# Kernel tuning notes

Measured on AMD Instinct MI355X. Metric: run time of the kernel, lower is better.

The kernel has to match this reference:

```python
import jax, jax.numpy as jnp
import numpy as np

B, NA, NK, E = 128, 1024, 10, 768
EPS = 1e-7


def setup_inputs() -> dict:
    k0 = jax.random.key(0)
    k1, k2, k3, k4 = jax.random.split(k0, 4)
    ans = jax.random.normal(k1, (B, NA, E), dtype=jnp.float32)
    key = jax.random.normal(k2, (B, NK, E), dtype=jnp.float32)
    # 0/1 padding masks; guarantee at least one valid token per row
    mask_ans = (jax.random.uniform(k3, (B, NA)) < 0.9).astype(jnp.float32)
    mask_ans = mask_ans.at[:, 0].set(1.0)
    mask_key = (jax.random.uniform(k4, (B, NK)) < 0.9).astype(jnp.float32)
    mask_key = mask_key.at[:, 0].set(1.0)
    return {"ans": ans, "mask_ans": mask_ans, "key": key, "mask_key": mask_key}


def reference(ans, mask_ans, key, mask_key):
    # additive -inf biases for padded positions, shaped [B,1,N]
    mask_ans_inf = (jnp.abs(mask_ans - 1.0) * -10000.0)[:, None, :]  # [B,1,NA]
    mask_key_inf = (jnp.abs(mask_key - 1.0) * -10000.0)[:, None, :]  # [B,1,NK]
    ans = ans * mask_ans[:, :, None]
    key = key * mask_key[:, :, None]

    # op == 'dp': raw dot-product scores, key x ans^T -> [B,NK,NA]
    Z = jnp.einsum('bke,bae->bka', key, ans)

    # cosine-normalized scores (intended math of the repeat_interleave/reshape)
    norm_ans = jnp.sqrt(jnp.maximum(jnp.sum(ans * ans, -1), EPS))  # [B,NA]
    norm_key = jnp.sqrt(jnp.maximum(jnp.sum(key * key, -1), EPS))  # [B,NK]
    Z_cos = Z / (norm_key[:, :, None] * norm_ans[:, None, :])      # [B,NK,NA]

    # key-direction attention: softmax over NK, aggregate key tokens per ans token
    Z_softmax_key = jax.nn.softmax(jnp.swapaxes(Z, 1, 2) + mask_key_inf, axis=2)  # [B,NA,NK]
    V = jnp.einsum('bak,bke->bae', Z_softmax_key, key) * mask_ans[:, :, None]     # [B,NA,E]

    # ans-direction attention: softmax over NA, aggregate ans tokens per key token
    Z_softmax_ans = jax.nn.softmax(Z + mask_ans_inf, axis=2)                      # [B,NK,NA]
    U = jnp.einsum('bka,bae->bke', Z_softmax_ans, ans) * mask_key[:, :, None]     # [B,NK,E]

    # sigmoid gating from best cosine match (temperature 5)
    beta_key = jax.nn.sigmoid(jnp.max(Z_cos + mask_ans_inf, axis=2) * 5.0)[:, :, None]  # [B,NK,1]
    beta_ans = jax.nn.sigmoid(
        jnp.max(jnp.swapaxes(Z_cos, 1, 2) + mask_key_inf, axis=2) * 5.0)[:, :, None]    # [B,NA,1]

    # beta == True
    U = U * beta_key
    V = V * beta_ans

    # word_att_pool == 'max'
    u = jnp.max(U, axis=1)  # [B,E]
    v = jnp.max(V, axis=1)  # [B,E]

    # merge_ans_key == 'concat'
    f = jnp.concatenate([u, v], axis=1)  # [B,2E]

    return (f, Z, Z_softmax_ans,
            jnp.swapaxes(Z_softmax_key, 1, 2),  # [B,NK,NA]
            jnp.swapaxes(beta_ans, 1, 2),       # [B,1,NA]
            jnp.swapaxes(beta_key, 1, 2))       # [B,1,NK]
```

## Files before the change

### kernel.cpp

```cpp
#include <hip/hip_runtime.h>
#include <math.h>

#define NB 128
#define NA 1024
#define NK 10
#define EDIM 768
#define NS 4
#define CHUNK (NA/NS)
#define WPB 4
#define TPB 256
#define TPW (CHUNK/WPB)
#define NG (TPW/4)
#define EPSV 1e-7f

#define F_OFF   0
#define Z_OFF   196608
#define ZSA_OFF 1507328
#define ZSK_OFF 2818048
#define BA_OFF  4128768
#define BK_OFF  4259840

#define WS_META (NK*EDIM + EDIM)
#define WS_STRIDE (WS_META + 32)

__device__ __forceinline__ float wave_sum(float v) {
#define DPPADD(ctrl) v += __int_as_float(__builtin_amdgcn_update_dpp(0, __float_as_int(v), ctrl, 0xf, 0xf, true))
  DPPADD(0x111); DPPADD(0x112); DPPADD(0x114); DPPADD(0x118);
  DPPADD(0x142); DPPADD(0x143);
#undef DPPADD
  return __int_as_float(__builtin_amdgcn_readlane(__float_as_int(v), 63));
}

__global__ __launch_bounds__(TPB, 1) void kv_pass1(
    const float* __restrict__ ans, const float* __restrict__ mask_ans,
    const float* __restrict__ key, const float* __restrict__ mask_key,
    float* __restrict__ out, float* __restrict__ ws)
{
  const int s = blockIdx.x, b = blockIdx.y;
  const int tid = threadIdx.x;
  const int lane = tid & 63, wave = tid >> 6;

  __shared__ float key_s[NK][EDIM];
  __shared__ float red_u[NK][EDIM];
  __shared__ float vred[WPB][EDIM];
  __shared__ float rnk_s[NK], mki_s[NK];
  __shared__ float shm[WPB][NK], shl[WPB][NK], shmc[WPB][NK];
  __shared__ float fm[NK];

  {
    const float* kb = key + (size_t)b*NK*EDIM;
    float* kd = &key_s[0][0];
    for (int i = tid*4; i < NK*EDIM; i += TPB*4) {
      float4 v = *(const float4*)(kb + i);
      float mk = mask_key[b*NK + (i / EDIM)];
      v.x*=mk; v.y*=mk; v.z*=mk; v.w*=mk;
      *(float4*)(kd + i) = v;
    }
  }
  __syncthreads();
  for (int k = wave; k < NK; k += WPB) {
    float ss = 0.f;
    for (int j = lane; j < EDIM; j += 64) { float t = key_s[k][j]; ss += t*t; }
    ss = wave_sum(ss);
    if (lane == 0) {
      rnk_s[k] = rsqrtf(fmaxf(ss, EPSV));
      mki_s[k] = (mask_key[b*NK + k] - 1.0f) * 10000.0f;
    }
  }
  __syncthreads();

  float Uacc[NK][12];
  float vmax[12];
  float m[NK], l[NK], mc[NK];
#pragma unroll
  for (int k = 0; k < NK; ++k) {
    m[k] = -1e30f; l[k] = 0.f; mc[k] = -3e38f;
#pragma unroll
    for (int j = 0; j < 12; ++j) Uacc[k][j] = 0.f;
  }
#pragma unroll
  for (int j = 0; j < 12; ++j) vmax[j] = -3e38f;

  const float* ansb = ans + (size_t)b*NA*EDIM;
  const int abase = s*CHUNK + wave*TPW;

#pragma unroll 1
  for (int g = 0; g < NG; ++g) {
    const int a0 = abase + g*4;
    float av[4][12];
    float ma[4], mainf[4], rna[4], bfac[4];
    float zz[4][NK];

#pragma unroll
    for (int t = 0; t < 4; ++t) {
      const int a = a0 + t;
      const float mav = mask_ans[b*NA + a];
      ma[t] = mav; mainf[t] = (mav - 1.0f)*10000.0f;
      float ns = 0.f;
#pragma unroll
      for (int j = 0; j < 3; ++j) {
        float4 v = *(const float4*)(ansb + (size_t)a*EDIM + j*256 + lane*4);
        v.x*=mav; v.y*=mav; v.z*=mav; v.w*=mav;
        av[t][j*4+0]=v.x; av[t][j*4+1]=v.y; av[t][j*4+2]=v.z; av[t][j*4+3]=v.w;
        ns += v.x*v.x + v.y*v.y + v.z*v.z + v.w*v.w;
      }
      ns = wave_sum(ns);
      rna[t] = rsqrtf(fmaxf(ns, EPSV));
    }

#pragma unroll
    for (int k = 0; k < NK; ++k) {
      float kb0[12];
#pragma unroll
      for (int j = 0; j < 3; ++j) {
        float4 v = *(const float4*)(&key_s[k][j*256 + lane*4]);
        kb0[j*4+0]=v.x; kb0[j*4+1]=v.y; kb0[j*4+2]=v.z; kb0[j*4+3]=v.w;
      }
#pragma unroll
      for (int t = 0; t < 4; ++t) {
        float p = 0.f;
#pragma unroll
        for (int j = 0; j < 12; ++j) p += av[t][j]*kb0[j];
        zz[t][k] = p;
      }
    }
#pragma unroll
    for (int t = 0; t < 4; ++t)
#pragma unroll
      for (int k = 0; k < NK; ++k) zz[t][k] = wave_sum(zz[t][k]);

    float w[4][NK];
#pragma unroll
    for (int t = 0; t < 4; ++t) {
      const int a = a0 + t;
      {
        float zv = zz[t][0];
#pragma unroll
        for (int k = 1; k < NK; ++k) zv = (lane == k) ? zz[t][k] : zv;
        if (lane < NK) out[Z_OFF + ((size_t)b*NK + lane)*NA + a] = zv;
      }
      float mk = zz[t][0] + mki_s[0];
#pragma unroll
      for (int k = 1; k < NK; ++k) mk = fmaxf(mk, zz[t][k] + mki_s[k]);
      float sum = 0.f;
#pragma unroll
      for (int k = 0; k < NK; ++k) { float e = __expf(zz[t][k] + mki_s[k] - mk); w[t][k] = e; sum += e; }
      float rs = 1.0f / sum;
#pragma unroll
      for (int k = 0; k < NK; ++k) w[t][k] *= rs;
      {
        float wv = w[t][0];
#pragma unroll
        for (int k = 1; k < NK; ++k) wv = (lane == k) ? w[t][k] : wv;
        if (lane < NK) out[ZSK_OFF + ((size_t)b*NK + lane)*NA + a] = wv;
      }
      float zc0 = zz[t][0]*rnk_s[0]*rna[t];
      float cb = zc0 + mki_s[0];
      mc[0] = fmaxf(mc[0], zc0 + mainf[t]);
#pragma unroll
      for (int k = 1; k < NK; ++k) {
        float zc = zz[t][k]*rnk_s[k]*rna[t];
        cb = fmaxf(cb, zc + mki_s[k]);
        mc[k] = fmaxf(mc[k], zc + mainf[t]);
      }
      float beta = 1.0f / (1.0f + __expf(-5.0f*cb));
      if (lane == 0) out[BA_OFF + (size_t)b*NA + a] = beta;
      bfac[t] = beta * ma[t];
#pragma unroll
      for (int k = 0; k < NK; ++k) {
        float sc = zz[t][k] + mainf[t];
        if (sc > m[k]) {
          float scale = __expf(m[k] - sc);
          m[k] = sc; l[k] *= scale;
#pragma unroll
          for (int j = 0; j < 12; ++j) Uacc[k][j] *= scale;
        }
        float p = __expf(sc - m[k]);
        l[k] += p;
#pragma unroll
        for (int j = 0; j < 12; ++j) Uacc[k][j] += p * av[t][j];
      }
    }

    float Vv[4][12];
#pragma unroll
    for (int t = 0; t < 4; ++t)
#pragma unroll
      for (int j = 0; j < 12; ++j) Vv[t][j] = 0.f;
#pragma unroll
    for (int k = 0; k < NK; ++k) {
      float kb0[12];
#pragma unroll
      for (int j = 0; j < 3; ++j) {
        float4 v = *(const float4*)(&key_s[k][j*256 + lane*4]);
        kb0[j*4+0]=v.x; kb0[j*4+1]=v.y; kb0[j*4+2]=v.z; kb0[j*4+3]=v.w;
      }
#pragma unroll
      for (int t = 0; t < 4; ++t)
#pragma unroll
        for (int j = 0; j < 12; ++j) Vv[t][j] += w[t][k]*kb0[j];
    }
#pragma unroll
    for (int t = 0; t < 4; ++t)
#pragma unroll
      for (int j = 0; j < 12; ++j) vmax[j] = fmaxf(vmax[j], Vv[t][j]*bfac[t]);
  }

  if (lane == 0) {
#pragma unroll
    for (int k = 0; k < NK; ++k) { shm[wave][k]=m[k]; shl[wave][k]=l[k]; shmc[wave][k]=mc[k]; }
  }
#pragma unroll
  for (int j = 0; j < 12; ++j) vred[wave][(j>>2)*256 + lane*4 + (j&3)] = vmax[j];
  for (int i = tid; i < NK*EDIM; i += TPB) (&red_u[0][0])[i] = 0.f;
  __syncthreads();

  float* wsb = ws + (size_t)(b*NS + s)*WS_STRIDE;
  if (tid < NK) {
    const int k = tid;
    float M = shm[0][k];
#pragma unroll
    for (int w2 = 1; w2 < WPB; ++w2) M = fmaxf(M, shm[w2][k]);
    float L = 0.f, MC = shmc[0][k];
#pragma unroll
    for (int w2 = 0; w2 < WPB; ++w2) {
      L += shl[w2][k]*__expf(shm[w2][k]-M);
      MC = fmaxf(MC, shmc[w2][k]);
    }
    fm[k] = M;
    wsb[WS_META + k] = M;
    wsb[WS_META + NK + k] = L;
    wsb[WS_META + 2*NK + k] = MC;
  }
  __syncthreads();
#pragma unroll
  for (int k = 0; k < NK; ++k) {
    float fw = __expf(m[k] - fm[k]);
#pragma unroll
    for (int j = 0; j < 12; ++j)
      atomicAdd(&red_u[k][(j>>2)*256 + lane*4 + (j&3)], fw*Uacc[k][j]);
  }
  __syncthreads();
  for (int i = tid; i < NK*EDIM; i += TPB) wsb[i] = (&red_u[0][0])[i];
  for (int i = tid; i < EDIM; i += TPB)
    wsb[NK*EDIM + i] = fmaxf(fmaxf(vred[0][i], vred[1][i]), fmaxf(vred[2][i], vred[3][i]));
}

__global__ __launch_bounds__(256, 1) void kv_pass2(
    const float* __restrict__ mask_ans, const float* __restrict__ mask_key,
    float* __restrict__ out, const float* __restrict__ ws)
{
  const int b = blockIdx.x, tid = threadIdx.x;
  __shared__ float shM[NK], shRL[NK], shFac[NK], shF[NS][NK];
  if (tid < NK) {
    const int k = tid;
    const float* w0 = ws + (size_t)(b*NS)*WS_STRIDE + WS_META;
    float M = w0[k];
#pragma unroll
    for (int s2 = 1; s2 < NS; ++s2) M = fmaxf(M, w0[(size_t)s2*WS_STRIDE + k]);
    float L = 0.f, MC = -3e38f;
#pragma unroll
    for (int s2 = 0; s2 < NS; ++s2) {
      float ms = w0[(size_t)s2*WS_STRIDE + k];
      float f = __expf(ms - M);
      shF[s2][k] = f;
      L  += w0[(size_t)s2*WS_STRIDE + NK + k] * f;
      MC  = fmaxf(MC, w0[(size_t)s2*WS_STRIDE + 2*NK + k]);
    }
    float bk = 1.0f/(1.0f + __expf(-5.0f*MC));
    out[BK_OFF + b*NK + k] = bk;
    float rl = 1.0f / L;
    shM[k] = M; shRL[k] = rl;
    shFac[k] = rl * mask_key[b*NK + k] * bk;
  }
  __syncthreads();
  const float* wsb = ws + (size_t)(b*NS)*WS_STRIDE;
#pragma unroll 1
  for (int e = tid; e < EDIM; e += 256) {
    float u = -3e38f;
#pragma unroll
    for (int k = 0; k < NK; ++k) {
      float acc = 0.f;
#pragma unroll
      for (int s2 = 0; s2 < NS; ++s2) acc += shF[s2][k] * wsb[(size_t)s2*WS_STRIDE + k*EDIM + e];
      u = fmaxf(u, acc * shFac[k]);
    }
    out[(size_t)b*(2*EDIM) + e] = u;
    float v = wsb[NK*EDIM + e];
#pragma unroll
    for (int s2 = 1; s2 < NS; ++s2) v = fmaxf(v, wsb[(size_t)s2*WS_STRIDE + NK*EDIM + e]);
    out[(size_t)b*(2*EDIM) + EDIM + e] = v;
  }
  for (int i = tid; i < NK*NA; i += 256) {
    const int a = i & (NA-1);
    const int k = i >> 10;
    float z = out[Z_OFF + (size_t)b*NK*NA + i];
    float mainf = (mask_ans[b*NA + a] - 1.0f) * 10000.0f;
    out[ZSA_OFF + (size_t)b*NK*NA + i] = __expf(z + mainf - shM[k]) * shRL[k];
  }
}

extern "C" void kernel_launch(void* const* d_in, const int* in_sizes, int n_in,
                              void* d_out, int out_size, void* d_ws, size_t ws_size,
                              hipStream_t stream) {
  const float* ans      = (const float*)d_in[0];
  const float* mask_ans = (const float*)d_in[1];
  const float* key      = (const float*)d_in[2];
  const float* mask_key = (const float*)d_in[3];
  float* out = (float*)d_out;
  float* ws  = (float*)d_ws;

  dim3 g1(NS, NB);
  kv_pass1<<<g1, TPB, 0, stream>>>(ans, mask_ans, key, mask_key, out, ws);
  kv_pass2<<<NB, 256, 0, stream>>>(mask_ans, mask_key, out, ws);
}
```

Measured before the change: 1.467 ms.

## Move ans-direction softmax aggregation out of online loop into separate third pass

```diff
diff --git a/kernel.cpp b/kernel.cpp
--- a/kernel.cpp
+++ b/kernel.cpp
@@ -10,7 +10,6 @@
 #define WPB 4
 #define TPB 256
 #define TPW (CHUNK/WPB)
-#define NG (TPW/4)
 #define EPSV 1e-7f
 
 #define F_OFF   0
@@ -20,8 +19,10 @@
 #define BA_OFF  4128768
 #define BK_OFF  4259840
 
-#define WS_META (NK*EDIM + EDIM)
-#define WS_STRIDE (WS_META + 32)
+#define WS_RNK 0
+#define WS_RNA (WS_RNK + NB*NK)
+#define WS_VP  (WS_RNA + NB*NA)
+#define WS_FAC (WS_VP + NB*NS*EDIM)
 
 __device__ __forceinline__ float wave_sum(float v) {
 #define DPPADD(ctrl) v += __int_as_float(__builtin_amdgcn_update_dpp(0, __float_as_int(v), ctrl, 0xf, 0xf, true))
@@ -30,8 +31,15 @@
 #undef DPPADD
   return __int_as_float(__builtin_amdgcn_readlane(__float_as_int(v), 63));
 }
-
-__global__ __launch_bounds__(TPB, 1) void kv_pass1(
+__device__ __forceinline__ float wave_max(float v) {
+#define DPPMAX(ctrl) { float o_ = __int_as_float(__builtin_amdgcn_update_dpp(__float_as_int(v), __float_as_int(v), ctrl, 0xf, 0xf, false)); v = fmaxf(v, o_); }
+  DPPMAX(0x111) DPPMAX(0x112) DPPMAX(0x114) DPPMAX(0x118)
+  DPPMAX(0x142) DPPMAX(0x143)
+#undef DPPMAX
+  return __int_as_float(__builtin_amdgcn_readlane(__float_as_int(v), 63));
+}
+
+__global__ __launch_bounds__(TPB, 2) void kv_pass1(
     const float* __restrict__ ans, const float* __restrict__ mask_ans,
     const float* __restrict__ key, const float* __restrict__ mask_key,
     float* __restrict__ out, float* __restrict__ ws)
@@ -41,43 +49,33 @@
   const int lane = tid & 63, wave = tid >> 6;
 
   __shared__ float key_s[NK][EDIM];
-  __shared__ float red_u[NK][EDIM];
   __shared__ float vred[WPB][EDIM];
   __shared__ float rnk_s[NK], mki_s[NK];
-  __shared__ float shm[WPB][NK], shl[WPB][NK], shmc[WPB][NK];
-  __shared__ float fm[NK];
 
   {
     const float* kb = key + (size_t)b*NK*EDIM;
-    float* kd = &key_s[0][0];
     for (int i = tid*4; i < NK*EDIM; i += TPB*4) {
       float4 v = *(const float4*)(kb + i);
       float mk = mask_key[b*NK + (i / EDIM)];
       v.x*=mk; v.y*=mk; v.z*=mk; v.w*=mk;
-      *(float4*)(kd + i) = v;
+      *(float4*)(&key_s[0][0] + i) = v;
     }
   }
   __syncthreads();
   for (int k = wave; k < NK; k += WPB) {
-    float ss = 0.f;
-    for (int j = lane; j < EDIM; j += 64) { float t = key_s[k][j]; ss += t*t; }
-    ss = wave_sum(ss);
+    float ssum = 0.f;
+    for (int j = lane; j < EDIM; j += 64) { float t = key_s[k][j]; ssum += t*t; }
+    ssum = wave_sum(ssum);
     if (lane == 0) {
-      rnk_s[k] = rsqrtf(fmaxf(ss, EPSV));
+      float r = rsqrtf(fmaxf(ssum, EPSV));
+      rnk_s[k] = r;
       mki_s[k] = (mask_key[b*NK + k] - 1.0f) * 10000.0f;
-    }
-  }
-  __syncthreads();
-
-  float Uacc[NK][12];
+      if (s == 0) ws[WS_RNK + b*NK + k] = r;
+    }
+  }
+  __syncthreads();
+
   float vmax[12];
-  float m[NK], l[NK], mc[NK];
-#pragma unroll
-  for (int k = 0; k < NK; ++k) {
-    m[k] = -1e30f; l[k] = 0.f; mc[k] = -3e38f;
-#pragma unroll
-    for (int j = 0; j < 12; ++j) Uacc[k][j] = 0.f;
-  }
 #pragma unroll
   for (int j = 0; j < 12; ++j) vmax[j] = -3e38f;
 
@@ -85,17 +83,16 @@
   const int abase = s*CHUNK + wave*TPW;
 
 #pragma unroll 1
-  for (int g = 0; g < NG; ++g) {
-    const int a0 = abase + g*4;
-    float av[4][12];
-    float ma[4], mainf[4], rna[4], bfac[4];
-    float zz[4][NK];
-
-#pragma unroll
-    for (int t = 0; t < 4; ++t) {
+  for (int g = 0; g < TPW/2; ++g) {
+    const int a0 = abase + g*2;
+    float av[2][12], rna2[2], ma2[2], bfac[2];
+    float zz[2][NK], w[2][NK];
+
+#pragma unroll
+    for (int t = 0; t < 2; ++t) {
       const int a = a0 + t;
       const float mav = mask_ans[b*NA + a];
-      ma[t] = mav; mainf[t] = (mav - 1.0f)*10000.0f;
+      ma2[t] = mav;
       float ns = 0.f;
 #pragma unroll
       for (int j = 0; j < 3; ++j) {
@@ -105,43 +102,40 @@
         ns += v.x*v.x + v.y*v.y + v.z*v.z + v.w*v.w;
       }
       ns = wave_sum(ns);
-      rna[t] = rsqrtf(fmaxf(ns, EPSV));
+      rna2[t] = rsqrtf(fmaxf(ns, EPSV));
+      if (lane == 0) ws[WS_RNA + b*NA + a] = rna2[t];
     }
 
 #pragma unroll
     for (int k = 0; k < NK; ++k) {
-      float kb0[12];
+      float kr[12];
 #pragma unroll
       for (int j = 0; j < 3; ++j) {
         float4 v = *(const float4*)(&key_s[k][j*256 + lane*4]);
-        kb0[j*4+0]=v.x; kb0[j*4+1]=v.y; kb0[j*4+2]=v.z; kb0[j*4+3]=v.w;
-      }
-#pragma unroll
-      for (int t = 0; t < 4; ++t) {
-        float p = 0.f;
-#pragma unroll
-        for (int j = 0; j < 12; ++j) p += av[t][j]*kb0[j];
-        zz[t][k] = p;
-      }
-    }
-#pragma unroll
-    for (int t = 0; t < 4; ++t)
+        kr[j*4+0]=v.x; kr[j*4+1]=v.y; kr[j*4+2]=v.z; kr[j*4+3]=v.w;
+      }
+      float p0 = 0.f, p1 = 0.f;
+#pragma unroll
+      for (int j = 0; j < 12; ++j) { p0 += av[0][j]*kr[j]; p1 += av[1][j]*kr[j]; }
+      zz[0][k] = p0; zz[1][k] = p1;
+    }
+#pragma unroll
+    for (int t = 0; t < 2; ++t)
 #pragma unroll
       for (int k = 0; k < NK; ++k) zz[t][k] = wave_sum(zz[t][k]);
 
-    float w[4][NK];
-#pragma unroll
-    for (int t = 0; t < 4; ++t) {
+#pragma unroll
+    for (int t = 0; t < 2; ++t) {
       const int a = a0 + t;
       {
         float zv = zz[t][0];
 #pragma unroll
         for (int k = 1; k < NK; ++k) zv = (lane == k) ? zz[t][k] : zv;
-        if (lane < NK) out[Z_OFF + ((size_t)b*NK + lane)*NA + a] = zv;
-      }
-      float mk = zz[t][0] + mki_s[0];
-#pragma unroll
-      for (int k = 1; k < NK; ++k) mk = fmaxf(mk, zz[t][k] + mki_s[k]);
+        if (lane < NK) out[Z_OFF + ((size_t)(b*NK) + lane)*NA + a] = zv;
+      }
+      float mk = -3e38f;
+#pragma unroll
+      for (int k = 0; k < NK; ++k) mk = fmaxf(mk, zz[t][k] + mki_s[k]);
       float sum = 0.f;
 #pragma unroll
       for (int k = 0; k < NK; ++k) { float e = __expf(zz[t][k] + mki_s[k] - mk); w[t][k] = e; sum += e; }
@@ -152,152 +146,133 @@
         float wv = w[t][0];
 #pragma unroll
         for (int k = 1; k < NK; ++k) wv = (lane == k) ? w[t][k] : wv;
-        if (lane < NK) out[ZSK_OFF + ((size_t)b*NK + lane)*NA + a] = wv;
-      }
-      float zc0 = zz[t][0]*rnk_s[0]*rna[t];
-      float cb = zc0 + mki_s[0];
-      mc[0] = fmaxf(mc[0], zc0 + mainf[t]);
-#pragma unroll
-      for (int k = 1; k < NK; ++k) {
-        float zc = zz[t][k]*rnk_s[k]*rna[t];
-        cb = fmaxf(cb, zc + mki_s[k]);
-        mc[k] = fmaxf(mc[k], zc + mainf[t]);
-      }
+        if (lane < NK) out[ZSK_OFF + ((size_t)(b*NK) + lane)*NA + a] = wv;
+      }
+      float cb = -3e38f;
+#pragma unroll
+      for (int k = 0; k < NK; ++k) cb = fmaxf(cb, zz[t][k]*rnk_s[k]*rna2[t] + mki_s[k]);
       float beta = 1.0f / (1.0f + __expf(-5.0f*cb));
       if (lane == 0) out[BA_OFF + (size_t)b*NA + a] = beta;
-      bfac[t] = beta * ma[t];
-#pragma unroll
-      for (int k = 0; k < NK; ++k) {
-        float sc = zz[t][k] + mainf[t];
-        if (sc > m[k]) {
-          float scale = __expf(m[k] - sc);
-          m[k] = sc; l[k] *= scale;
-#pragma unroll
-          for (int j = 0; j < 12; ++j) Uacc[k][j] *= scale;
-        }
-        float p = __expf(sc - m[k]);
-        l[k] += p;
-#pragma unroll
-        for (int j = 0; j < 12; ++j) Uacc[k][j] += p * av[t][j];
-      }
-    }
-
-    float Vv[4][12];
-#pragma unroll
-    for (int t = 0; t < 4; ++t)
+      bfac[t] = beta * ma2[t];
+    }
+
+    float Vv[2][12];
+#pragma unroll
+    for (int t = 0; t < 2; ++t)
 #pragma unroll
       for (int j = 0; j < 12; ++j) Vv[t][j] = 0.f;
 #pragma unroll
     for (int k = 0; k < NK; ++k) {
-      float kb0[12];
+      float kr[12];
 #pragma unroll
       for (int j = 0; j < 3; ++j) {
         float4 v = *(const float4*)(&key_s[k][j*256 + lane*4]);
-        kb0[j*4+0]=v.x; kb0[j*4+1]=v.y; kb0[j*4+2]=v.z; kb0[j*4+3]=v.w;
-      }
-#pragma unroll
-      for (int t = 0; t < 4; ++t)
-#pragma unroll
-        for (int j = 0; j < 12; ++j) Vv[t][j] += w[t][k]*kb0[j];
-    }
-#pragma unroll
-    for (int t = 0; t < 4; ++t)
+        kr[j*4+0]=v.x; kr[j*4+1]=v.y; kr[j*4+2]=v.z; kr[j*4+3]=v.w;
+      }
+#pragma unroll
+      for (int t = 0; t < 2; ++t)
+#pragma unroll
+        for (int j = 0; j < 12; ++j) Vv[t][j] += w[t][k]*kr[j];
+    }
+#pragma unroll
+    for (int t = 0; t < 2; ++t)
 #pragma unroll
       for (int j = 0; j < 12; ++j) vmax[j] = fmaxf(vmax[j], Vv[t][j]*bfac[t]);
   }
 
-  if (lane == 0) {
-#pragma unroll
-    for (int k = 0; k < NK; ++k) { shm[wave][k]=m[k]; shl[wave][k]=l[k]; shmc[wave][k]=mc[k]; }
-  }
-#pragma unroll
-  for (int j = 0; j < 12; ++j) vred[wave][(j>>2)*256 + lane*4 + (j&3)] = vmax[j];
-  for (int i = tid; i < NK*EDIM; i += TPB) (&red_u[0][0])[i] = 0.f;
-  __syncthreads();
-
-  float* wsb = ws + (size_t)(b*NS + s)*WS_STRIDE;
-  if (tid < NK) {
-    const int k = tid;
-    float M = shm[0][k];
-#pragma unroll
-    for (int w2 = 1; w2 < WPB; ++w2) M = fmaxf(M, shm[w2][k]);
-    float L = 0.f, MC = shmc[0][k];
-#pragma unroll
-    for (int w2 = 0; w2 < WPB; ++w2) {
-      L += shl[w2][k]*__expf(shm[w2][k]-M);
-      MC = fmaxf(MC, shmc[w2][k]);
-    }
-    fm[k] = M;
-    wsb[WS_META + k] = M;
-    wsb[WS_META + NK + k] = L;
-    wsb[WS_META + 2*NK + k] = MC;
-  }
-  __syncthreads();
-#pragma unroll
-  for (int k = 0; k < NK; ++k) {
-    float fw = __expf(m[k] - fm[k]);
-#pragma unroll
-    for (int j = 0; j < 12; ++j)
-      atomicAdd(&red_u[k][(j>>2)*256 + lane*4 + (j&3)], fw*Uacc[k][j]);
-  }
-  __syncthreads();
-  for (int i = tid; i < NK*EDIM; i += TPB) wsb[i] = (&red_u[0][0])[i];
+#pragma unroll
+  for (int j = 0; j < 3; ++j)
+    *(float4*)(&vred[wave][j*256 + lane*4]) =
+      make_float4(vmax[j*4+0], vmax[j*4+1], vmax[j*4+2], vmax[j*4+3]);
+  __syncthreads();
   for (int i = tid; i < EDIM; i += TPB)
-    wsb[NK*EDIM + i] = fmaxf(fmaxf(vred[0][i], vred[1][i]), fmaxf(vred[2][i], vred[3][i]));
-}
-
-__global__ __launch_bounds__(256, 1) void kv_pass2(
+    ws[WS_VP + ((size_t)(b*NS + s))*EDIM + i] =
+      fmaxf(fmaxf(vred[0][i], vred[1][i]), fmaxf(vred[2][i], vred[3][i]));
+}
+
+__global__ __launch_bounds__(256, 2) void kv_pass2(
     const float* __restrict__ mask_ans, const float* __restrict__ mask_key,
-    float* __restrict__ out, const float* __restrict__ ws)
+    float* __restrict__ out, float* __restrict__ ws)
 {
   const int b = blockIdx.x, tid = threadIdx.x;
-  __shared__ float shM[NK], shRL[NK], shFac[NK], shF[NS][NK];
+  const int lane = tid & 63, wave = tid >> 6;
+  __shared__ float shM[NK], shRL[NK], shMC[NK];
+
+  float mainf16[16], rna16[16];
+#pragma unroll
+  for (int i = 0; i < 16; ++i) {
+    int a = i*64 + lane;
+    mainf16[i] = (mask_ans[b*NA + a] - 1.0f) * 10000.0f;
+    rna16[i]   = ws[WS_RNA + b*NA + a];
+  }
+  for (int k = wave; k < NK; k += 4) {
+    float rnk = ws[WS_RNK + b*NK + k];
+    float z16[16];
+    float M = -3e38f, MC = -3e38f;
+#pragma unroll
+    for (int i = 0; i < 16; ++i) {
+      float z = out[Z_OFF + ((size_t)(b*NK) + k)*NA + i*64 + lane];
+      z16[i] = z;
+      M  = fmaxf(M,  z + mainf16[i]);
+      MC = fmaxf(MC, z*rnk*rna16[i] + mainf16[i]);
+    }
+    M = wave_max(M); MC = wave_max(MC);
+    float L = 0.f;
+#pragma unroll
+    for (int i = 0; i < 16; ++i) L += __expf(z16[i] + mainf16[i] - M);
+    L = wave_sum(L);
+    if (lane == 0) { shM[k] = M; shRL[k] = 1.0f/L; shMC[k] = MC; }
+  }
+  __syncthreads();
   if (tid < NK) {
-    const int k = tid;
-    const float* w0 = ws + (size_t)(b*NS)*WS_STRIDE + WS_META;
-    float M = w0[k];
-#pragma unroll
-    for (int s2 = 1; s2 < NS; ++s2) M = fmaxf(M, w0[(size_t)s2*WS_STRIDE + k]);
-    float L = 0.f, MC = -3e38f;
-#pragma unroll
-    for (int s2 = 0; s2 < NS; ++s2) {
-      float ms = w0[(size_t)s2*WS_STRIDE + k];
-      float f = __expf(ms - M);
-      shF[s2][k] = f;
-      L  += w0[(size_t)s2*WS_STRIDE + NK + k] * f;
-      MC  = fmaxf(MC, w0[(size_t)s2*WS_STRIDE + 2*NK + k]);
-    }
-    float bk = 1.0f/(1.0f + __expf(-5.0f*MC));
-    out[BK_OFF + b*NK + k] = bk;
-    float rl = 1.0f / L;
-    shM[k] = M; shRL[k] = rl;
-    shFac[k] = rl * mask_key[b*NK + k] * bk;
-  }
-  __syncthreads();
-  const float* wsb = ws + (size_t)(b*NS)*WS_STRIDE;
-#pragma unroll 1
-  for (int e = tid; e < EDIM; e += 256) {
-    float u = -3e38f;
-#pragma unroll
-    for (int k = 0; k < NK; ++k) {
-      float acc = 0.f;
-#pragma unroll
-      for (int s2 = 0; s2 < NS; ++s2) acc += shF[s2][k] * wsb[(size_t)s2*WS_STRIDE + k*EDIM + e];
-      u = fmaxf(u, acc * shFac[k]);
-    }
-    out[(size_t)b*(2*EDIM) + e] = u;
-    float v = wsb[NK*EDIM + e];
-#pragma unroll
-    for (int s2 = 1; s2 < NS; ++s2) v = fmaxf(v, wsb[(size_t)s2*WS_STRIDE + NK*EDIM + e]);
-    out[(size_t)b*(2*EDIM) + EDIM + e] = v;
+    float bk = 1.0f / (1.0f + __expf(-5.0f*shMC[tid]));
+    out[BK_OFF + b*NK + tid] = bk;
+    ws[WS_FAC + b*NK + tid] = bk * mask_key[b*NK + tid];
   }
   for (int i = tid; i < NK*NA; i += 256) {
-    const int a = i & (NA-1);
-    const int k = i >> 10;
+    int k = i >> 10, a = i & (NA-1);
     float z = out[Z_OFF + (size_t)b*NK*NA + i];
     float mainf = (mask_ans[b*NA + a] - 1.0f) * 10000.0f;
     out[ZSA_OFF + (size_t)b*NK*NA + i] = __expf(z + mainf - shM[k]) * shRL[k];
   }
+  {
+    const float* vp = ws + WS_VP + (size_t)b*NS*EDIM;
+    for (int e = tid; e < EDIM; e += 256) {
+      float v = vp[e];
+#pragma unroll
+      for (int s2 = 1; s2 < NS; ++s2) v = fmaxf(v, vp[s2*EDIM + e]);
+      out[(size_t)b*2*EDIM + EDIM + e] = v;
+    }
+  }
+}
+
+__global__ __launch_bounds__(192) void kv_pass3(
+    const float* __restrict__ ans, float* out, const float* __restrict__ ws)
+{
+  const int es = blockIdx.x, b = blockIdx.y, tid = threadIdx.x;
+  const int e = es*192 + tid;
+  const float* zsa = out + ZSA_OFF + (size_t)b*NK*NA;
+  const float* ap  = ans + (size_t)b*NA*EDIM + e;
+  float acc[NK];
+#pragma unroll
+  for (int k = 0; k < NK; ++k) acc[k] = 0.f;
+
+#pragma unroll 1
+  for (int a0 = 0; a0 < NA; a0 += 8) {
+    float av[8];
+#pragma unroll
+    for (int t = 0; t < 8; ++t) av[t] = ap[(size_t)(a0 + t)*EDIM];
+#pragma unroll
+    for (int k = 0; k < NK; ++k) {
+#pragma unroll
+      for (int t = 0; t < 8; ++t) acc[k] += zsa[k*NA + a0 + t] * av[t];
+    }
+  }
+  float u = -3e38f;
+  const float* fac = ws + WS_FAC + b*NK;
+#pragma unroll
+  for (int k = 0; k < NK; ++k) u = fmaxf(u, acc[k]*fac[k]);
+  out[(size_t)b*2*EDIM + e] = u;
 }
 
 extern "C" void kernel_launch(void* const* d_in, const int* in_sizes, int n_in,
@@ -313,4 +288,6 @@
   dim3 g1(NS, NB);
   kv_pass1<<<g1, TPB, 0, stream>>>(ans, mask_ans, key, mask_key, out, ws);
   kv_pass2<<<NB, 256, 0, stream>>>(mask_ans, mask_key, out, ws);
-}
+  dim3 g3(4, NB);
+  kv_pass3<<<g3, 192, 0, stream>>>(ans, out, ws);
+}
```

Result: faster. 1.349 ms (-8.1%).
